# Performance work log

Measured on AMD Instinct MI355X. Metric: run time of the kernel, lower is better.

The kernel has to match this reference:

```python
import jax, jax.numpy as jnp
import numpy as np
from jax import lax

B = 2048


def setup_inputs() -> dict:
    key = jax.random.key(0)
    ks = jax.random.split(key, 12)
    r = lambda k, s, sc=0.05: jax.random.normal(k, s, jnp.float32) * sc
    return {
        "w": jax.random.normal(ks[0], (B, 512), jnp.float32),
        "init_const": r(ks[1], (1, 512, 4, 4), 0.1),
        "init_conv_w": r(ks[2], (256, 512, 3, 3)),
        "init_conv_b": r(ks[3], (256,)),
        "aff1_w": r(ks[4], (256, 512)),
        "aff1_b": r(ks[5], (256,)),
        "conv1_w": r(ks[6], (128, 256, 3, 3)),
        "conv1_b": r(ks[7], (128,)),
        "aff2_w": r(ks[8], (128, 512)),
        "aff2_b": r(ks[9], (128,)),
        "conv2_w": r(ks[10], (64, 128, 3, 3)),
        "conv2_b": r(ks[11], (64,)),
    }


def _conv3(x, W):
    # 3x3 conv, stride 1, padding 1, NCHW / OIHW
    return lax.conv_general_dilated(x, W, (1, 1), ((1, 1), (1, 1)),
                                    dimension_numbers=("NCHW", "OIHW", "NCHW"))


def _lrelu(x):
    return jnp.where(x >= 0, x, 0.2 * x)


def reference(w, init_const, init_conv_w, init_conv_b,
              aff1_w, aff1_b, conv1_w, conv1_b,
              aff2_w, aff2_b, conv2_w, conv2_b):
    batch = w.shape[0]
    x = _conv3(init_const, init_conv_w) + init_conv_b[None, :, None, None]
    x = _lrelu(x)                                   # [1,256,4,4]
    x = jnp.broadcast_to(x, (batch,) + x.shape[1:])  # repeat over batch
    layers = ((aff1_w, aff1_b, conv1_w, conv1_b),
              (aff2_w, aff2_b, conv2_w, conv2_b))
    for aw, ab, cw, cb in layers:
        b_, c, h, wd = x.shape
        # bilinear upsample x2 (half-pixel centers == torch align_corners=False)
        x = jax.image.resize(x, (b_, c, 2 * h, 2 * wd), "bilinear")
        style = w @ aw.T + ab                        # [B, Cin]
        # modulated conv: conv(s*x, W) * demod, where
        # demod[b,o] = rsqrt(sum_{c,k} (s[b,c] W[o,c,k])^2 + 1e-8)
        xm = x * style[:, :, None, None]
        y = _conv3(xm, cw)                           # [B, Cout, 2h, 2w]
        w2 = jnp.sum(cw * cw, axis=(2, 3))           # [Cout, Cin]
        demod = lax.rsqrt(jnp.einsum("bc,oc->bo", style * style, w2) + 1e-8)
        x = _lrelu(y * demod[:, :, None, None] + cb[None, :, None, None])
    return x
```

## Files before the change

kernel.cpp:

```cpp
#include <hip/hip_runtime.h>
#include <hip/hip_fp16.h>

typedef _Float16 f16x8 __attribute__((ext_vector_type(8)));
typedef float f32x4 __attribute__((ext_vector_type(4)));

#define WS_X0U   0
#define WS_GHP   65536
#define WS_W2P   4259840
#define WS_WH    4407296
#define WS_AFTH  6504448
#define WS_W2TH  6897664
#define WS_S1P   7045120
#define WS_S2H   8093696
#define WS_SSQ   8617984
#define WS_D1    10190848
#define WS_D2    11239424
#define WS_X1T   11763712

__device__ __forceinline__ void up_wi(int j, int S, int& i0, int& i1,
                                      float& w0, float& w1) {
  int m = j >> 1;
  if (j & 1) { i0 = m; i1 = (m + 1 < S) ? m + 1 : S - 1; w0 = 0.75f; w1 = 0.25f; }
  else       { i0 = (m - 1 >= 0) ? m - 1 : 0; i1 = m;     w0 = 0.25f; w1 = 0.75f; }
}

__device__ __forceinline__ int xq_off(int pix, int i) {
  return (pix >> 1) * 64 + (((((pix & 1) << 2) + i) ^ ((pix >> 1) & 7)) << 3);
}

__global__ __launch_bounds__(256) void k_pre0(const float* __restrict__ ic,
    const float* __restrict__ w0c, const float* __restrict__ b0,
    const float* __restrict__ w1c, const float* __restrict__ w2c,
    const float* __restrict__ a1w, const float* __restrict__ a2w,
    const float* __restrict__ wsrc,
    float* __restrict__ x0u, _Float16* __restrict__ w2p,
    _Float16* __restrict__ wh, _Float16* __restrict__ afTh,
    _Float16* __restrict__ W2Th) {
  __shared__ float xl[512 * 16];
  __shared__ float part[16 * 257];
  __shared__ float part2[16 * 17];
  __shared__ float x4[16];
  int t = threadIdx.x;
  if (blockIdx.x < 256) {
    int o = blockIdx.x;
    for (int i = t; i < 512 * 16; i += 256) xl[i] = ic[i];
    __syncthreads();
    float acc[16];
#pragma unroll
    for (int p = 0; p < 16; ++p) acc[p] = 0.f;
#pragma unroll
    for (int it = 0; it < 18; ++it) {
      int j = it * 256 + t;
      float wv = w0c[o * 4608 + j];
      int c = j / 9, k = j - c * 9;
      int dy = k / 3, dx = k - dy * 3;
      const float* xc = &xl[c * 16];
#pragma unroll
      for (int p = 0; p < 16; ++p) {
        int py = p >> 2, px = p & 3;
        int iy = py + dy - 1, ix = px + dx - 1;
        bool ok = ((unsigned)iy < 4u) && ((unsigned)ix < 4u);
        float xv = ok ? xc[iy * 4 + ix] : 0.f;
        acc[p] += wv * xv;
      }
    }
#pragma unroll
    for (int p = 0; p < 16; ++p) part[p * 257 + t] = acc[p];
    __syncthreads();
    {
      int p = t & 15, ch = t >> 4;
      float s = 0.f;
#pragma unroll
      for (int g = 0; g < 16; ++g) s += part[p * 257 + ch * 16 + g];
      part2[p * 17 + ch] = s;
    }
    __syncthreads();
    if (t < 16) {
      float v = b0[t == 0 ? o : o];
      v = b0[o];
      float s = v;
#pragma unroll
      for (int g = 0; g < 16; ++g) s += part2[t * 17 + g];
      x4[t] = (s >= 0.f) ? s : 0.2f * s;
    }
    __syncthreads();
    if (t < 64) {
      int oy = t >> 3, ox = t & 7;
      int y0, y1, xx0, xx1; float wy0, wy1, wx0, wx1;
      up_wi(oy, 4, y0, y1, wy0, wy1);
      up_wi(ox, 4, xx0, xx1, wx0, wx1);
      float v = wy0 * (wx0 * x4[y0 * 4 + xx0] + wx1 * x4[y0 * 4 + xx1])
              + wy1 * (wx0 * x4[y1 * 4 + xx0] + wx1 * x4[y1 * 4 + xx1]);
      x0u[o * 64 + t] = v;
    }
  } else {
    int idx = (blockIdx.x - 256) * 256 + t;
    if (idx < 73728) {
      int tap = idx / 8192, r = idx & 8191;
      int kg = r >> 11, mf = (r >> 9) & 3, l = (r >> 3) & 63, j = r & 7;
      int o = mf * 16 + (l & 15);
      int c = kg * 32 + (l >> 4) * 8 + j;
      w2p[idx] = (_Float16)w2c[(o * 128 + c) * 9 + tap];
    } else if (idx < 73728 + 1048576) {
      int i = idx - 73728;
      wh[i] = (_Float16)wsrc[i];
    } else if (idx < 73728 + 1048576 + 196608) {
      int i = idx - 73728 - 1048576;
      afTh[i] = (_Float16)((i < 131072) ? a1w[i] : a2w[i - 131072]);
    } else if (idx < 73728 + 1048576 + 196608 + 73728) {
      int i = idx - 73728 - 1048576 - 196608;
      int o = i / 384, k = i - o * 384;
      float v = 0.f;
      const float* wp = nullptr;
      if (o < 128 && k < 256)        wp = w1c + (o * 256 + k) * 9;
      else if (o >= 128 && k >= 256) wp = w2c + ((o - 128) * 128 + (k - 256)) * 9;
      if (wp) {
#pragma unroll
        for (int q = 0; q < 9; ++q) v += wp[q] * wp[q];
      }
      W2Th[i] = (_Float16)v;
    }
  }
}

__global__ __launch_bounds__(256) void k_pre1(const float* __restrict__ w1c,
    const float* __restrict__ x0u, _Float16* __restrict__ Ghp,
    const _Float16* __restrict__ wh, const _Float16* __restrict__ afTh,
    const float* __restrict__ a1b, const float* __restrict__ a2b,
    _Float16* __restrict__ s1p, _Float16* __restrict__ s2h,
    _Float16* __restrict__ ssq) {
  __shared__ _Float16 x0l[256][66];
  int t = threadIdx.x;
  if (blockIdx.x < 512) {
    int o = blockIdx.x >> 2, pg = blockIdx.x & 3;
    for (int i = t; i < 256 * 64; i += 256) {
      int c = i >> 6, p = i & 63;
      x0l[c][p] = (_Float16)x0u[i];
    }
    __syncthreads();
    int c = t;
    float wr9[9];
#pragma unroll
    for (int k = 0; k < 9; ++k) wr9[k] = w1c[(o * 256 + c) * 9 + k];
    int cpart = ((((c >> 3) & 3) * 16 + (o & 15)) * 8) + (c & 7);
    int cq = c >> 5, oq = o >> 4;
    for (int p = pg * 16; p < pg * 16 + 16; ++p) {
      int py = p >> 3, px = p & 7;
      float acc = 0.f;
#pragma unroll
      for (int dy = 0; dy < 3; ++dy) {
        int iy = py + dy - 1;
        if ((unsigned)iy >= 8u) continue;
#pragma unroll
        for (int dx = 0; dx < 3; ++dx) {
          int ix = px + dx - 1;
          if ((unsigned)ix >= 8u) continue;
          acc += wr9[dy * 3 + dx] * (float)x0l[c][iy * 8 + ix];
        }
      }
      Ghp[((p * 8 + oq) * 8 + cq) * 512 + cpart] = (_Float16)acc;
    }
  } else {
    int i = blockIdx.x - 512;
    int sx = i % 6, sy = i / 6;
    int lane = t & 63, w = t >> 6;
    int wr = w >> 1, wc = w & 1;
    int b0 = sy * 64 + wr * 32;
    int f0 = sx * 64 + wc * 32;
    f32x4 acc[2][2] = {};
    int lr = lane & 15, lk = (lane >> 4) * 8;
#pragma unroll
    for (int kg = 0; kg < 16; ++kg) {
      f16x8 af[2], bf[2];
#pragma unroll
      for (int mf = 0; mf < 2; ++mf)
        af[mf] = *(const f16x8*)(wh + (b0 + mf * 16 + lr) * 512 + kg * 32 + lk);
#pragma unroll
      for (int nf = 0; nf < 2; ++nf)
        bf[nf] = *(const f16x8*)(afTh + (f0 + nf * 16 + lr) * 512 + kg * 32 + lk);
#pragma unroll
      for (int mf = 0; mf < 2; ++mf)
#pragma unroll
        for (int nf = 0; nf < 2; ++nf)
          acc[mf][nf] = __builtin_amdgcn_mfma_f32_16x16x32_f16(af[mf], bf[nf], acc[mf][nf], 0, 0, 0);
    }
    int r4 = lane >> 4;
#pragma unroll
    for (int nf = 0; nf < 2; ++nf) {
      int f = f0 + nf * 16 + lr;
      float bias = (f < 256) ? a1b[f] : a2b[f - 256];
#pragma unroll
      for (int mf = 0; mf < 2; ++mf) {
#pragma unroll
        for (int r = 0; r < 4; ++r) {
          int b = b0 + mf * 16 + r4 * 4 + r;
          float v = acc[mf][nf][r] + bias;
          ssq[b * 384 + f] = (_Float16)(v * v);
          if (f < 256) {
            int flat = (((b >> 4) * 8 + (f >> 5)) * 64 + ((f >> 3) & 3) * 16 + (b & 15)) * 8 + (f & 7);
            s1p[flat] = (_Float16)v;
          } else {
            s2h[b * 128 + (f - 256)] = (_Float16)v;
          }
        }
      }
    }
  }
}

__global__ __launch_bounds__(256) void k_dmd(const _Float16* __restrict__ ssq,
    const _Float16* __restrict__ W2Th, float* __restrict__ d1,
    float* __restrict__ d2) {
  int t = threadIdx.x, lane = t & 63, w = t >> 6;
  int wr = w >> 1, wc = w & 1;
  int b0 = blockIdx.y * 64 + wr * 32;
  int o0 = blockIdx.x * 64 + wc * 32;
  int kbeg = (blockIdx.x == 2) ? 8 : 0;
  int kend = (blockIdx.x == 2) ? 12 : 8;
  f32x4 acc[2][2] = {};
  int lr = lane & 15, lk = (lane >> 4) * 8;
  for (int kg = kbeg; kg < kend; ++kg) {
    f16x8 af[2], bf[2];
#pragma unroll
    for (int mf = 0; mf < 2; ++mf)
      af[mf] = *(const f16x8*)(ssq + (b0 + mf * 16 + lr) * 384 + kg * 32 + lk);
#pragma unroll
    for (int nf = 0; nf < 2; ++nf)
      bf[nf] = *(const f16x8*)(W2Th + (o0 + nf * 16 + lr) * 384 + kg * 32 + lk);
#pragma unroll
    for (int mf = 0; mf < 2; ++mf)
#pragma unroll
      for (int nf = 0; nf < 2; ++nf)
        acc[mf][nf] = __builtin_amdgcn_mfma_f32_16x16x32_f16(af[mf], bf[nf], acc[mf][nf], 0, 0, 0);
  }
  int r4 = lane >> 4;
#pragma unroll
  for (int mf = 0; mf < 2; ++mf) {
#pragma unroll
    for (int r = 0; r < 4; ++r) {
      int b = b0 + mf * 16 + r4 * 4 + r;
#pragma unroll
      for (int nf = 0; nf < 2; ++nf) {
        int o = o0 + nf * 16 + lr;
        float v = rsqrtf(acc[mf][nf][r] + 1e-8f);
        if (o < 128) d1[b * 128 + o] = v;
        else         d2[b * 64 + (o - 128)] = v;
      }
    }
  }
}

__global__ __launch_bounds__(256) void k_l1(const _Float16* __restrict__ s1p,
    const _Float16* __restrict__ Ghp, const float* __restrict__ d1,
    const float* __restrict__ c1b, const _Float16* __restrict__ s2h,
    __half* __restrict__ x1t) {
  int t = threadIdx.x, lane = t & 63, w = t >> 6;
  int wr = w >> 1, wc = w & 1;
  int bq0 = blockIdx.y * 8 + wr * 4;
  int nq0 = blockIdx.x * 8 + wc * 4;
  f32x4 acc[4][4] = {};
#pragma unroll
  for (int kg = 0; kg < 8; ++kg) {
    f16x8 af[4], bf[4];
#pragma unroll
    for (int mf = 0; mf < 4; ++mf)
      af[mf] = *(const f16x8*)(s1p + (((bq0 + mf) * 8 + kg) * 64 + lane) * 8);
#pragma unroll
    for (int nf = 0; nf < 4; ++nf)
      bf[nf] = *(const f16x8*)(Ghp + (((nq0 + nf) * 8 + kg) * 64 + lane) * 8);
#pragma unroll
    for (int mf = 0; mf < 4; ++mf)
#pragma unroll
      for (int nf = 0; nf < 4; ++nf)
        acc[mf][nf] = __builtin_amdgcn_mfma_f32_16x16x32_f16(af[mf], bf[nf], acc[mf][nf], 0, 0, 0);
  }
  int nc = lane & 15, r4 = lane >> 4;
#pragma unroll
  for (int mf = 0; mf < 4; ++mf) {
#pragma unroll
    for (int r = 0; r < 4; ++r) {
      int b = (bq0 + mf) * 16 + r4 * 4 + r;
#pragma unroll
      for (int nf = 0; nf < 4; ++nf) {
        int n = (nq0 + nf) * 16 + nc;
        int o = n & 127, p = n >> 7;
        float v = acc[mf][nf][r] * d1[b * 128 + o] + c1b[o];
        v = (v >= 0.f) ? v : 0.2f * v;
        v *= (float)s2h[b * 128 + o];
        x1t[(b * 64 + p) * 128 + o] = (__half)v;
      }
    }
  }
}

__global__ __launch_bounds__(256, 2) void k_l2(const __half* __restrict__ x1t,
    const float* __restrict__ d2g, const _Float16* __restrict__ w2p,
    const float* __restrict__ c2b, float* __restrict__ out) {
  int b = blockIdx.x, t = threadIdx.x;
  int lane = t & 63, w = t >> 6;
  __shared__ unsigned short xq[2][9792];
  __shared__ unsigned short x1l[64 * 128];
  const __half* xb = x1t + b * 8192;

  for (int idx = t; idx < 1024; idx += 256) {
    int q = idx >> 4, gc = idx & 15;
    f16x8 v = *(const f16x8*)(xb + q * 128 + gc * 8);
    int gs = (gc & 8) | ((gc ^ q) & 7);
    *(f16x8*)&x1l[q * 128 + gs * 8] = v;
  }
  {
    f16x8 z = {};
    for (int idx = t; idx < 400; idx += 256) {
      int pg = idx >> 3, g = idx & 7;
      int buf = g >> 2, i = g & 3;
      int pix;
      if (pg < 18) pix = 288 + pg;
      else { int j = pg - 18; pix = (j >> 1) * 18 + (j & 1) * 17; }
      *(f16x8*)&xq[buf][xq_off(pix, i)] = z;
    }
  }
  f16x8 afb[3][4];
#pragma unroll
  for (int mf = 0; mf < 4; ++mf) {
    afb[0][mf] = *(const f16x8*)(w2p + (((0 * 4 + 0) * 4 + mf) * 64 + lane) * 8);
    afb[1][mf] = *(const f16x8*)(w2p + (((3 * 4 + 0) * 4 + mf) * 64 + lane) * 8);
  }
  int fy = t >> 4, fx = t & 15;
  int y0, y1, x0, x1i; float wy0, wy1, wx0, wx1;
  up_wi(fy, 8, y0, y1, wy0, wy1);
  up_wi(fx, 8, x0, x1i, wx0, wx1);
  _Float16 wA = (_Float16)(wy0 * wx0), wB = (_Float16)(wy0 * wx1);
  _Float16 wC = (_Float16)(wy1 * wx0), wD = (_Float16)(wy1 * wx1);
  int pixb = fy * 18 + fx + 1;
  int q00 = y0 * 8 + x0, q01 = y0 * 8 + x1i, q10 = y1 * 8 + x0, q11 = y1 * 8 + x1i;

  auto build_granule = [&](int qn, int i) {
    int gc = qn * 4 + i;
    f16x8 va = *(const f16x8*)&x1l[q00 * 128 + ((gc & 8) | ((gc ^ q00) & 7)) * 8];
    f16x8 vb = *(const f16x8*)&x1l[q01 * 128 + ((gc & 8) | ((gc ^ q01) & 7)) * 8];
    f16x8 vc = *(const f16x8*)&x1l[q10 * 128 + ((gc & 8) | ((gc ^ q10) & 7)) * 8];
    f16x8 vd = *(const f16x8*)&x1l[q11 * 128 + ((gc & 8) | ((gc ^ q11) & 7)) * 8];
    f16x8 v = va * wA;
    v += vb * wB;
    v += vc * wC;
    v += vd * wD;
    *(f16x8*)&xq[qn & 1][xq_off(pixb, i)] = v;
  };

  __syncthreads();
#pragma unroll
  for (int i = 0; i < 4; ++i) build_granule(0, i);
  __syncthreads();

  f32x4 acc[4][4] = {};
  f16x8 rw[2][6];
  int ig = lane >> 4;
  int colb = lane & 15;

  auto read_win = [&](int qb, int buf, int dx) {
#pragma unroll
    for (int j = 0; j < 6; ++j) {
      int fr = w * 4 + j - 1;
      int srow = ((unsigned)fr < 16u) ? fr : 16;
      int pix = srow * 18 + colb + dx;
      rw[buf][j] = *(const f16x8*)&xq[qb][xq_off(pix, ig)];
    }
  };

#pragma unroll
  for (int q = 0; q < 4; ++q) {
    read_win(q & 1, 0, 0);
#pragma unroll
    for (int dx = 0; dx < 3; ++dx) {
      if (dx < 2) read_win(q & 1, (dx + 1) & 1, dx + 1);
      if (q < 3) {
        if (dx == 0) { build_granule(q + 1, 0); build_granule(q + 1, 1); }
        else if (dx == 1) build_granule(q + 1, 2);
        else              build_granule(q + 1, 3);
      }
#pragma unroll
      for (int dy = 0; dy < 3; ++dy) {
        const int u = q * 9 + dx * 3 + dy;
        if (u + 2 < 36) {
          const int un = u + 2;
          const int qn = un / 9, rn = un - qn * 9;
          const int dxn = rn / 3, dyn = rn - dxn * 3;
          const int tapn = dyn * 3 + dxn;
#pragma unroll
          for (int mf = 0; mf < 4; ++mf)
            afb[un % 3][mf] = *(const f16x8*)(w2p + (((tapn * 4 + qn) * 4 + mf) * 64 + lane) * 8);
        }
        __builtin_amdgcn_s_setprio(1);
#pragma unroll
        for (int mf = 0; mf < 4; ++mf)
#pragma unroll
          for (int nf = 0; nf < 4; ++nf)
            acc[mf][nf] = __builtin_amdgcn_mfma_f32_16x16x32_f16(afb[u % 3][mf], rw[dx & 1][nf + dy], acc[mf][nf], 0, 0, 0);
        __builtin_amdgcn_s_setprio(0);
      }
    }
    if (q < 3) __syncthreads();
  }
  int px = lane & 15, r4 = lane >> 4;
#pragma unroll
  for (int mf = 0; mf < 4; ++mf) {
#pragma unroll
    for (int r = 0; r < 4; ++r) {
      int o = mf * 16 + r4 * 4 + r;
      float dm = d2g[b * 64 + o], bias = c2b[o];
#pragma unroll
      for (int nf = 0; nf < 4; ++nf) {
        int py = w * 4 + nf;
        float v = acc[mf][nf][r] * dm + bias;
        v = (v >= 0.f) ? v : 0.2f * v;
        out[(b * 64 + o) * 256 + py * 16 + px] = v;
      }
    }
  }
}

extern "C" void kernel_launch(void* const* d_in, const int* in_sizes, int n_in,
                              void* d_out, int out_size, void* d_ws, size_t ws_size,
                              hipStream_t stream) {
  const float* w    = (const float*)d_in[0];
  const float* ic   = (const float*)d_in[1];
  const float* w0c  = (const float*)d_in[2];
  const float* b0   = (const float*)d_in[3];
  const float* a1w  = (const float*)d_in[4];
  const float* a1b  = (const float*)d_in[5];
  const float* w1c  = (const float*)d_in[6];
  const float* c1b  = (const float*)d_in[7];
  const float* a2w  = (const float*)d_in[8];
  const float* a2b  = (const float*)d_in[9];
  const float* w2c  = (const float*)d_in[10];
  const float* c2b  = (const float*)d_in[11];
  float* out = (float*)d_out;
  char* ws = (char*)d_ws;

  float*    x0u  = (float*)(ws + WS_X0U);
  _Float16* Ghp  = (_Float16*)(ws + WS_GHP);
  _Float16* w2p  = (_Float16*)(ws + WS_W2P);
  _Float16* wh   = (_Float16*)(ws + WS_WH);
  _Float16* afTh = (_Float16*)(ws + WS_AFTH);
  _Float16* W2Th = (_Float16*)(ws + WS_W2TH);
  _Float16* s1p  = (_Float16*)(ws + WS_S1P);
  _Float16* s2h  = (_Float16*)(ws + WS_S2H);
  _Float16* ssq  = (_Float16*)(ws + WS_SSQ);
  float*    d1   = (float*)(ws + WS_D1);
  float*    d2   = (float*)(ws + WS_D2);
  __half*   x1t  = (__half*)(ws + WS_X1T);

  k_pre0 <<<5696, 256, 0, stream>>>(ic, w0c, b0, w1c, w2c, a1w, a2w, w,
                                    x0u, w2p, wh, afTh, W2Th);
  k_pre1 <<<704, 256, 0, stream>>>(w1c, x0u, Ghp, wh, afTh, a1b, a2b,
                                   s1p, s2h, ssq);
  dim3 gd(3, 32);
  k_dmd  <<<gd, 256, 0, stream>>>(ssq, W2Th, d1, d2);
  dim3 g1(64, 16);
  k_l1   <<<g1, 256, 0, stream>>>(s1p, Ghp, d1, c1b, s2h, x1t);
  k_l2   <<<2048, 256, 0, stream>>>(x1t, d2, w2p, c2b, out);
}
```

Measured before the change: 140.6 us.

## Halve layer-2 staging LDS and raise occupancy to three blocks per CU

The layer-2 kernel now stages only half of the 128 input channels in LDS at a time. The second half is held in registers and written into LDS during the q==0 compute phase, after both granule sets for q0 and q1 have been built up front. The zero-padding row is shared between the two buffers so they shrink to 19008 halves, and launch bounds go from 2 to 3 blocks per CU. This cuts LDS use per block to allow more resident waves. In exchange it adds register pressure from the held half and a more complex reuse schedule for x1l.

Result: slower. 302.3 us (+115.0%).

```diff
diff --git a/kernel.cpp b/kernel.cpp
--- a/kernel.cpp
+++ b/kernel.cpp
@@ -76,9 +76,7 @@
     }
     __syncthreads();
     if (t < 16) {
-      float v = b0[t == 0 ? o : o];
-      v = b0[o];
-      float s = v;
+      float s = b0[o];
 #pragma unroll
       for (int g = 0; g < 16; ++g) s += part2[t * 17 + g];
       x4[t] = (s >= 0.f) ? s : 0.2f * s;
@@ -293,30 +291,36 @@
   }
 }
 
-__global__ __launch_bounds__(256, 2) void k_l2(const __half* __restrict__ x1t,
+__global__ __launch_bounds__(256, 3) void k_l2(const __half* __restrict__ x1t,
     const float* __restrict__ d2g, const _Float16* __restrict__ w2p,
     const float* __restrict__ c2b, float* __restrict__ out) {
   int b = blockIdx.x, t = threadIdx.x;
   int lane = t & 63, w = t >> 6;
-  __shared__ unsigned short xq[2][9792];
-  __shared__ unsigned short x1l[64 * 128];
+  __shared__ unsigned short xq_all[19008];
+  __shared__ unsigned short x1l[4096];
   const __half* xb = x1t + b * 8192;
 
-  for (int idx = t; idx < 1024; idx += 256) {
-    int q = idx >> 4, gc = idx & 15;
-    f16x8 v = *(const f16x8*)(xb + q * 128 + gc * 8);
-    int gs = (gc & 8) | ((gc ^ q) & 7);
-    *(f16x8*)&x1l[q * 128 + gs * 8] = v;
-  }
+  int q1 = t >> 3, g1 = t & 7;
+  f16x8 s0a = *(const f16x8*)(xb + q1 * 128 + g1 * 8);
+  f16x8 s0b = *(const f16x8*)(xb + (q1 + 32) * 128 + g1 * 8);
+  f16x8 h1a = *(const f16x8*)(xb + q1 * 128 + 64 + g1 * 8);
+  f16x8 h1b = *(const f16x8*)(xb + (q1 + 32) * 128 + 64 + g1 * 8);
+  *(f16x8*)&x1l[q1 * 64 + ((g1 ^ (q1 & 7)) << 3)] = s0a;
+  *(f16x8*)&x1l[(q1 + 32) * 64 + ((g1 ^ ((q1 + 32) & 7)) << 3)] = s0b;
+
   {
     f16x8 z = {};
-    for (int idx = t; idx < 400; idx += 256) {
-      int pg = idx >> 3, g = idx & 7;
-      int buf = g >> 2, i = g & 3;
-      int pix;
-      if (pg < 18) pix = 288 + pg;
-      else { int j = pg - 18; pix = (j >> 1) * 18 + (j & 1) * 17; }
-      *(f16x8*)&xq[buf][xq_off(pix, i)] = z;
+    for (int idx = t; idx < 328; idx += 256) {
+      if (idx < 72) {
+        int pg = idx >> 2, i = idx & 3;
+        *(f16x8*)&xq_all[xq_off(288 + pg, i)] = z;
+      } else {
+        int j = idx - 72;
+        int buf = j >> 7, rem = j & 127;
+        int r = rem >> 3, side = (rem >> 2) & 1, i = rem & 3;
+        int pix = r * 18 + side * 17;
+        *(f16x8*)&xq_all[buf * 9792 + xq_off(pix, i)] = z;
+      }
     }
   }
   f16x8 afb[3][4];
@@ -335,21 +339,23 @@
   int q00 = y0 * 8 + x0, q01 = y0 * 8 + x1i, q10 = y1 * 8 + x0, q11 = y1 * 8 + x1i;
 
   auto build_granule = [&](int qn, int i) {
-    int gc = qn * 4 + i;
-    f16x8 va = *(const f16x8*)&x1l[q00 * 128 + ((gc & 8) | ((gc ^ q00) & 7)) * 8];
-    f16x8 vb = *(const f16x8*)&x1l[q01 * 128 + ((gc & 8) | ((gc ^ q01) & 7)) * 8];
-    f16x8 vc = *(const f16x8*)&x1l[q10 * 128 + ((gc & 8) | ((gc ^ q10) & 7)) * 8];
-    f16x8 vd = *(const f16x8*)&x1l[q11 * 128 + ((gc & 8) | ((gc ^ q11) & 7)) * 8];
+    int lgc = (qn & 1) * 4 + i;
+    f16x8 va = *(const f16x8*)&x1l[q00 * 64 + ((lgc ^ (q00 & 7)) << 3)];
+    f16x8 vb = *(const f16x8*)&x1l[q01 * 64 + ((lgc ^ (q01 & 7)) << 3)];
+    f16x8 vc = *(const f16x8*)&x1l[q10 * 64 + ((lgc ^ (q10 & 7)) << 3)];
+    f16x8 vd = *(const f16x8*)&x1l[q11 * 64 + ((lgc ^ (q11 & 7)) << 3)];
     f16x8 v = va * wA;
     v += vb * wB;
     v += vc * wC;
     v += vd * wD;
-    *(f16x8*)&xq[qn & 1][xq_off(pixb, i)] = v;
+    *(f16x8*)&xq_all[(qn & 1) * 9792 + xq_off(pixb, i)] = v;
   };
 
   __syncthreads();
 #pragma unroll
   for (int i = 0; i < 4; ++i) build_granule(0, i);
+#pragma unroll
+  for (int i = 0; i < 4; ++i) build_granule(1, i);
   __syncthreads();
 
   f32x4 acc[4][4] = {};
@@ -361,9 +367,9 @@
 #pragma unroll
     for (int j = 0; j < 6; ++j) {
       int fr = w * 4 + j - 1;
-      int srow = ((unsigned)fr < 16u) ? fr : 16;
-      int pix = srow * 18 + colb + dx;
-      rw[buf][j] = *(const f16x8*)&xq[qb][xq_off(pix, ig)];
+      bool inb = (unsigned)fr < 16u;
+      int pix = (inb ? fr : 16) * 18 + colb + dx;
+      rw[buf][j] = *(const f16x8*)&xq_all[(inb ? qb * 9792 : 0) + xq_off(pix, ig)];
     }
   };
 
@@ -373,7 +379,12 @@
 #pragma unroll
     for (int dx = 0; dx < 3; ++dx) {
       if (dx < 2) read_win(q & 1, (dx + 1) & 1, dx + 1);
-      if (q < 3) {
+      if (q == 0) {
+        if (dx == 0)
+          *(f16x8*)&x1l[q1 * 64 + ((g1 ^ (q1 & 7)) << 3)] = h1a;
+        else if (dx == 1)
+          *(f16x8*)&x1l[(q1 + 32) * 64 + ((g1 ^ ((q1 + 32) & 7)) << 3)] = h1b;
+      } else if (q < 3) {
         if (dx == 0) { build_granule(q + 1, 0); build_granule(q + 1, 1); }
         else if (dx == 1) build_granule(q + 1, 2);
         else              build_granule(q + 1, 3);
```
